# Performance work log

Hardware: AMD Instinct MI355X
Metric: run time of the kernel (lower is better)

## Reference

```python
import jax, jax.numpy as jnp
import numpy as np
from jax import lax


def setup_inputs() -> dict:
    key = jax.random.key(0)
    k0, k1, k2, k3 = jax.random.split(key, 4)
    B, Ct, Ht, Wt = 8, 16, 16, 16
    Cm, Hm, Wm = 16, 128, 128
    Cout, K = 64, 3
    template = jax.random.normal(k0, (B, Ct, Ht, Wt), jnp.float32)
    tomatch = jax.random.normal(k1, (B, Cm, Hm, Wm), jnp.float32)
    fan_in = Ct * Cm * K * K
    bound = 1.0 / np.sqrt(fan_in)
    W = jax.random.uniform(k2, (Cout, Ct * Cm, K, K), jnp.float32, -bound, bound)
    b = jax.random.uniform(k3, (Cout,), jnp.float32, -bound, bound)
    return {"template": template, "tomatch": tomatch, "W": W, "b": b}


def _dense_corr(template, tomatch):
    # template: [B, Ct, Ht, Wt], tomatch: [B, Cm, Hm, Wm]
    B, Ct, Ht, Wt = template.shape
    _, Cm, Hm, Wm = tomatch.shape
    # ReplicationPad2d((0, Wt-1, 0, Ht-1)) -> edge pad right/bottom only
    padded = jnp.pad(tomatch, ((0, 0), (0, 0), (0, Ht - 1), (0, Wt - 1)), mode="edge")

    def per_example(tm_pad, tp):
        # tm_pad: [Cm, Hm+Ht-1, Wm+Wt-1] -> treat Cm as batch with 1 channel
        # tp: [Ct, Ht, Wt] -> Ct single-channel filters
        out = lax.conv_general_dilated(
            tm_pad[:, None, :, :],  # [Cm, 1, Hp, Wp] NCHW
            tp[:, None, :, :],      # [Ct, 1, Ht, Wt] OIHW
            window_strides=(1, 1),
            padding="VALID",
        )  # [Cm, Ct, Hm, Wm] (torch conv2d = cross-correlation, same as lax)
        return out.reshape(Cm * Ct, Hm, Wm)  # channel = cm*Ct + ct, matches torch .view

    return jax.vmap(per_example)(padded, template)  # [B, Cm*Ct, Hm, Wm]


def reference(template, tomatch, W, b):
    corr = _dense_corr(template, tomatch)  # [B, Cm*Ct, Hm, Wm]
    out = lax.conv_general_dilated(corr, W, (1, 1), "SAME")  # 3x3 'same' merge conv
    return out + b[None, :, None, None]
```

## Files before the change

kernel.cpp:

```cpp
#include <hip/hip_runtime.h>
#include <hip/hip_bf16.h>


typedef __attribute__((ext_vector_type(4))) float  f32x4;
typedef __attribute__((ext_vector_type(8))) short  bf16x8;

__device__ inline unsigned int pack_bf16x2(float a, float b) {
    unsigned int ua = __builtin_bit_cast(unsigned int, a);
    unsigned int ub = __builtin_bit_cast(unsigned int, b);
    ua = (ua + 0x7fffu + ((ua >> 16) & 1u)) >> 16;
    ub = (ub + 0x7fffu + ((ub >> 16) & 1u)) >> 16;
    return ua | (ub << 16);
}
__device__ inline unsigned short cvt1(float f) {
    unsigned int u = __builtin_bit_cast(unsigned int, f);
    return (unsigned short)((u + 0x7fffu + ((u >> 16) & 1u)) >> 16);
}

__global__ __launch_bounds__(256) void corr_mfma(
    const float* __restrict__ tp, const float* __restrict__ tm,
    unsigned short* __restrict__ corrb)
{
    __shared__ __align__(16) unsigned short smA[2 * 2 * 31 * 82];

    const int t    = threadIdx.x;
    const int wave = t >> 6, lane = t & 63;
    const int n    = lane & 15, quad = lane >> 4;
    const int qh   = quad >> 1, jq = quad & 1;

    const int xh   = (int)blockIdx.x & 1;
    const int y0   = ((int)blockIdx.x >> 1) << 4;
    const int pair = (int)blockIdx.y & 7;
    const int b    = (int)blockIdx.y >> 3;
    const int xg0  = xh << 6;

    for (int cm2 = 0; cm2 < 2; ++cm2) {
        const float* src = tm + (((size_t)(b * 16 + pair * 2 + cm2)) << 14);
        for (int e = t; e < 31 * 80; e += 256) {
            int r = e / 80, c = e - r * 80;
            int gy = y0 + r;  gy = gy > 127 ? 127 : gy;
            int gx = xg0 + c; gx = gx > 127 ? 127 : gx;
            unsigned short h = cvt1(src[(gy << 7) + gx]);
            smA[((cm2 * 2 + 0) * 31 + r) * 82 + c] = h;
            if (c > 0)
                smA[((cm2 * 2 + 1) * 31 + r) * 82 + (c - 1)] = h;
        }
    }
    __syncthreads();

    bf16x8 bq[8];
    {
        const float* tpb = tp + (((size_t)(b * 16 + n)) << 8);
#pragma unroll
        for (int kc = 0; kc < 8; ++kc) {
            const float4* q = (const float4*)(tpb + (((2 * kc + qh) << 4) + (jq << 3)));
            float4 a = q[0], c4 = q[1];
            union { uint4 u; bf16x8 h; } cv;
            cv.u.x = pack_bf16x2(a.x, a.y);
            cv.u.y = pack_bf16x2(a.z, a.w);
            cv.u.z = pack_bf16x2(c4.x, c4.y);
            cv.u.w = pack_bf16x2(c4.z, c4.w);
            bq[kc] = cv.h;
        }
    }

    const unsigned* smAd = (const unsigned*)smA;
    const int PITCH = 41, PLANE = 31 * 41;

#pragma unroll 1
    for (int it = 0; it < 8; ++it) {
        const int lxa  = (wave << 4) + (it << 1);
        const int D00  = (n + qh) * PITCH + ((lxa + (jq << 3)) >> 1);

        f32x4 acc[4];
#pragma unroll
        for (int q = 0; q < 4; ++q) acc[q] = (f32x4){0.f, 0.f, 0.f, 0.f};

#pragma unroll
        for (int kc = 0; kc < 8; ++kc) {
            const int dof = D00 + kc * 82;
#pragma unroll
            for (int ch = 0; ch < 4; ++ch) {
                const int d = dof + ch * PLANE;
                union { uint4 u; bf16x8 h; } fr;
                fr.u.x = smAd[d];     fr.u.y = smAd[d + 1];
                fr.u.z = smAd[d + 2]; fr.u.w = smAd[d + 3];
                const int ai = ((ch & 1) << 1) | (ch >> 1);
                acc[ai] = __builtin_amdgcn_mfma_f32_16x16x32_bf16(
                    bq[kc], fr.h, acc[ai], 0, 0, 0);
            }
        }

        const int y = y0 + n;
#pragma unroll
        for (int ai = 0; ai < 4; ++ai) {
            const int par = ai >> 1, cm2 = ai & 1;
            const int x   = xg0 + lxa + par;
            uint2 v;
            v.x = pack_bf16x2(acc[ai][0], acc[ai][1]);
            v.y = pack_bf16x2(acc[ai][2], acc[ai][3]);
            unsigned short* dst = corrb
                + (((size_t)(b * 16384 + (y << 7) + x)) << 8)
                + (pair << 5) + (cm2 << 4) + (quad << 2);
            *(uint2*)dst = v;
        }
    }
}

__global__ __launch_bounds__(256) void wt_kernel(
    const float* __restrict__ W, unsigned short* __restrict__ Wb)
{
    int idx = (int)blockIdx.x * 256 + (int)threadIdx.x;
    int c  = idx & 255;
    int rem = idx >> 8;
    int co = rem % 64;
    int kk = rem / 64;
    Wb[idx] = cvt1(W[(size_t)co * 2304 + (size_t)c * 9 + kk]);
}

__global__ __launch_bounds__(256) void merge_mfma(
    const unsigned short* __restrict__ corrb, const unsigned short* __restrict__ Wb,
    const float* __restrict__ bias, float* __restrict__ out)
{
    __shared__ __align__(16) unsigned short sm[10 * 34 * 72];

    const int t    = threadIdx.x;
    const int wave = t >> 6, lane = t & 63;
    const int n    = lane & 15, quad = lane >> 4;
    const int x0   = (int)blockIdx.x << 5;
    const int y0   = (int)blockIdx.y << 3;
    const int b    = (int)blockIdx.z;

    f32x4 acc[4][4];
#pragma unroll
    for (int a = 0; a < 4; ++a)
#pragma unroll
        for (int q = 0; q < 4; ++q) acc[a][q] = (f32x4){0.f, 0.f, 0.f, 0.f};

    const unsigned short* cb = corrb + ((size_t)b << 22);

    uint4 v[11];

#define SLAB_LOAD(C0)                                                        \
    {                                                                        \
        _Pragma("unroll")                                                    \
        for (int k = 0; k < 11; ++k) {                                       \
            int e = t + (k << 8);                                            \
            int ci = e & 7, rem = e >> 3;                                    \
            int cc = rem % 34, r = rem / 34;                                 \
            int gy = y0 - 1 + r, gx = x0 - 1 + cc;                           \
            uint4 vv = {0u, 0u, 0u, 0u};                                     \
            if (e < 2720 && (unsigned)gy < 128u && (unsigned)gx < 128u)      \
                vv = *(const uint4*)(cb + (((size_t)((gy << 7) + gx)) << 8)  \
                                        + (C0) + (ci << 3));                 \
            v[k] = vv;                                                       \
        }                                                                    \
    }
#define SLAB_WRITE()                                                         \
    {                                                                        \
        _Pragma("unroll")                                                    \
        for (int k = 0; k < 11; ++k) {                                       \
            int e = t + (k << 8);                                            \
            int ci = e & 7, rem = e >> 3;                                    \
            int cc = rem % 34, r = rem / 34;                                 \
            if (e < 2720)                                                    \
                *(uint4*)&sm[r * 2448 + cc * 72 + (ci << 3)] = v[k];         \
        }                                                                    \
    }

    SLAB_LOAD(0)
    SLAB_WRITE()
    __syncthreads();

#pragma unroll 1
    for (int c0 = 0; c0 < 256; c0 += 64) {
        if (c0 < 192) SLAB_LOAD(c0 + 64)

        const unsigned short* wpb = Wb + (size_t)n * 256 + c0 + (quad << 3);
        bf16x8 afc[4];
        {
#pragma unroll
            for (int ct = 0; ct < 4; ++ct)
                afc[ct] = *(const bf16x8*)(wpb + (size_t)ct * 4096);
        }
#pragma unroll 1
        for (int idx = 0; idx < 18; ++idx) {
            const int nidx = idx < 17 ? idx + 1 : 17;
            const int nkk = nidx >> 1, nkc = nidx & 1;
            bf16x8 afn[4];
#pragma unroll
            for (int ct = 0; ct < 4; ++ct)
                afn[ct] = *(const bf16x8*)(wpb + (size_t)nkk * 16384
                                               + (nkc << 5) + (size_t)ct * 4096);
            const int kk = idx >> 1, kc = idx & 1;
            const int dy = kk / 3, dx = kk - 3 * dy;
#pragma unroll
            for (int nt = 0; nt < 4; ++nt) {
                const int prow = 2 * wave + (nt >> 1) + dy;
                const int pcol = ((nt & 1) << 4) + n + dx;
                bf16x8 bf = *(const bf16x8*)&sm[prow * 2448 + pcol * 72
                                                + (kc << 5) + (quad << 3)];
#pragma unroll
                for (int ct = 0; ct < 4; ++ct)
                    acc[ct][nt] = __builtin_amdgcn_mfma_f32_16x16x32_bf16(
                        afc[ct], bf, acc[ct][nt], 0, 0, 0);
            }
#pragma unroll
            for (int ct = 0; ct < 4; ++ct) afc[ct] = afn[ct];
        }

        __syncthreads();
        if (c0 < 192) SLAB_WRITE()
        __syncthreads();
    }

#pragma unroll
    for (int ct = 0; ct < 4; ++ct) {
#pragma unroll
        for (int nt = 0; nt < 4; ++nt) {
            const int y   = y0 + 2 * wave + (nt >> 1);
            const int x   = x0 + ((nt & 1) << 4) + n;
            const int co0 = (ct << 4) + (quad << 2);
            float* op = out + (((size_t)((b << 6) + co0) << 7) + y) * 128 + x;
#pragma unroll
            for (int r = 0; r < 4; ++r)
                op[(size_t)r << 14] = acc[ct][nt][r] + bias[co0 + r];
        }
    }
#undef SLAB_LOAD
#undef SLAB_WRITE
}

extern "C" void kernel_launch(void* const* d_in, const int* in_sizes, int n_in,
                              void* d_out, int out_size, void* d_ws, size_t ws_size,
                              hipStream_t stream)
{
    const float* tp   = (const float*)d_in[0];
    const float* tm   = (const float*)d_in[1];
    const float* Wt   = (const float*)d_in[2];
    const float* bias = (const float*)d_in[3];
    float* out = (float*)d_out;

    unsigned short* corrb = (unsigned short*)d_ws;
    unsigned short* Wb    = corrb + (size_t)8 * 16384 * 256;

    corr_mfma<<<dim3(16, 64), dim3(256), 0, stream>>>(tp, tm, corrb);
    wt_kernel<<<dim3(576), dim3(256), 0, stream>>>(Wt, Wb);
    merge_mfma<<<dim3(4, 16, 8), dim3(256), 0, stream>>>(corrb, Wb, bias, out);
}
```

Measured before the change: 194.1 us.

## Pre-pad tomatch into bf16 shifted planes and shrink merge tile

Adds a prep kernel that writes tomatch as edge-padded bf16 planes, with two column-parity copies, into workspace. A new correlation kernel then reads MFMA B fragments straight from global memory instead of staging through LDS. The merge kernel drops its register-prefetched double buffering for a smaller 16-wide tile with twice as many blocks, and the weight layout is reorganised for contiguous per-lane loads. This trades extra global traffic and an extra launch for fewer LDS stages and higher occupancy, and falls back to the old correlation path when the workspace is too small.

```diff
diff --git a/kernel.cpp b/kernel.cpp
--- a/kernel.cpp
+++ b/kernel.cpp
@@ -15,6 +15,191 @@
 __device__ inline unsigned short cvt1(float f) {
     unsigned int u = __builtin_bit_cast(unsigned int, f);
     return (unsigned short)((u + 0x7fffu + ((u >> 16) & 1u)) >> 16);
+}
+__device__ inline bf16x8 load16_a4(const unsigned short* p) {
+    bf16x8 v;
+    __builtin_memcpy(&v, __builtin_assume_aligned(p, 4), 16);
+    return v;
+}
+
+__global__ __launch_bounds__(256) void tmb_prep(
+    const float* __restrict__ tm, unsigned short* __restrict__ tmb)
+{
+    int idx = (int)blockIdx.x * 256 + (int)threadIdx.x;
+    int c   = idx % 144;
+    int rem = idx / 144;
+    int r   = rem % 143;  rem /= 143;
+    int cm  = rem & 15;   rem >>= 4;
+    int b   = rem & 7;
+    int p   = rem >> 3;
+    int gy = r > 127 ? 127 : r;
+    int gx = c + p; gx = gx > 127 ? 127 : gx;
+    tmb[idx] = cvt1(tm[(((size_t)(b * 16 + cm)) << 14) + (gy << 7) + gx]);
+}
+
+__global__ __launch_bounds__(256) void corr_g(
+    const float* __restrict__ tp, const unsigned short* __restrict__ tmb,
+    unsigned short* __restrict__ corrb)
+{
+    const int t    = threadIdx.x;
+    const int wave = t >> 6, lane = t & 63;
+    const int n    = lane & 15, quad = lane >> 4;
+    const int qh   = quad >> 1, jq = quad & 1;
+
+    const int y    = ((int)blockIdx.x << 2) + wave;
+    const int pair = (int)blockIdx.y & 7;
+    const int b    = (int)blockIdx.y >> 3;
+
+    bf16x8 bq[8];
+    {
+        const float* tpb = tp + (((size_t)(b * 16 + n)) << 8);
+#pragma unroll
+        for (int kc = 0; kc < 8; ++kc) {
+            const float4* q = (const float4*)(tpb + (((2 * kc + qh) << 4) + (jq << 3)));
+            float4 a = q[0], c4 = q[1];
+            union { uint4 u; bf16x8 h; } cv;
+            cv.u.x = pack_bf16x2(a.x, a.y);
+            cv.u.y = pack_bf16x2(a.z, a.w);
+            cv.u.z = pack_bf16x2(c4.x, c4.y);
+            cv.u.w = pack_bf16x2(c4.z, c4.w);
+            bq[kc] = cv.h;
+        }
+    }
+
+    const size_t PLANE = 20592;
+    const size_t PARS  = 128 * PLANE;
+    const size_t bcm0  = (size_t)(b * 16 + pair * 2) * PLANE;
+    const int    colb  = (n << 3) + (jq << 3);
+
+    f32x4 acc[2][8];
+#pragma unroll
+    for (int c2 = 0; c2 < 2; ++c2)
+#pragma unroll
+        for (int s = 0; s < 8; ++s) acc[c2][s] = (f32x4){0.f, 0.f, 0.f, 0.f};
+
+#pragma unroll 1
+    for (int kc = 0; kc < 8; ++kc) {
+        const int row = y + 2 * kc + qh;
+#pragma unroll
+        for (int c2 = 0; c2 < 2; ++c2) {
+            const unsigned short* base =
+                tmb + bcm0 + (size_t)c2 * PLANE + (size_t)row * 144 + colb;
+#pragma unroll
+            for (int s = 0; s < 8; ++s) {
+                const unsigned short* ps = base + (s & 1) * PARS + ((s >> 1) << 1);
+                bf16x8 bf = load16_a4(ps);
+                acc[c2][s] = __builtin_amdgcn_mfma_f32_16x16x32_bf16(
+                    bq[kc], bf, acc[c2][s], 0, 0, 0);
+            }
+        }
+    }
+
+    const size_t posb = ((size_t)(b * 16384 + (y << 7)) << 8) + (pair << 5);
+#pragma unroll
+    for (int s = 0; s < 8; ++s) {
+        const int x = (n << 3) + s;
+#pragma unroll
+        for (int c2 = 0; c2 < 2; ++c2) {
+            uint2 v;
+            v.x = pack_bf16x2(acc[c2][s][0], acc[c2][s][1]);
+            v.y = pack_bf16x2(acc[c2][s][2], acc[c2][s][3]);
+            *(uint2*)(corrb + posb + ((size_t)x << 8) + (c2 << 4) + (quad << 2)) = v;
+        }
+    }
+}
+
+__global__ __launch_bounds__(256) void wt_kernel(
+    const float* __restrict__ W, unsigned short* __restrict__ Wb2)
+{
+    int idx = (int)blockIdx.x * 256 + (int)threadIdx.x;
+    int ci = idx & 7;
+    int co = (idx >> 3) & 63;
+    int cb = (idx >> 9) & 31;
+    int kk = idx >> 14;
+    int c  = (cb << 3) + ci;
+    Wb2[idx] = cvt1(W[(size_t)co * 2304 + (size_t)c * 9 + kk]);
+}
+
+__global__ __launch_bounds__(256, 4) void merge_mfma(
+    const unsigned short* __restrict__ corrb, const unsigned short* __restrict__ Wb2,
+    const float* __restrict__ bias, float* __restrict__ out)
+{
+    __shared__ __align__(16) unsigned short sm[10 * 18 * 72];
+
+    const int t    = threadIdx.x;
+    const int wave = t >> 6, lane = t & 63;
+    const int n    = lane & 15, quad = lane >> 4;
+    const int x0   = (int)blockIdx.x << 4;
+    const int y0   = (int)blockIdx.y << 3;
+    const int b    = (int)blockIdx.z;
+
+    f32x4 acc[4][2];
+#pragma unroll
+    for (int a = 0; a < 4; ++a)
+#pragma unroll
+        for (int q = 0; q < 2; ++q) acc[a][q] = (f32x4){0.f, 0.f, 0.f, 0.f};
+
+    const unsigned short* cb = corrb + ((size_t)b << 22);
+
+#pragma unroll 1
+    for (int c0 = 0; c0 < 256; c0 += 64) {
+        __syncthreads();
+#pragma unroll
+        for (int k = 0; k < 6; ++k) {
+            int e = t + (k << 8);
+            if (e < 1440) {
+                int ci  = e & 7;
+                int rem = e >> 3;
+                int cc  = rem % 18, r = rem / 18;
+                int gy = y0 - 1 + r, gx = x0 - 1 + cc;
+                uint4 vv = {0u, 0u, 0u, 0u};
+                if ((unsigned)gy < 128u && (unsigned)gx < 128u)
+                    vv = *(const uint4*)(cb + (((size_t)((gy << 7) + gx)) << 8)
+                                            + c0 + (ci << 3));
+                *(uint4*)&sm[(r * 18 + cc) * 72 + (ci << 3)] = vv;
+            }
+        }
+        __syncthreads();
+
+#pragma unroll 1
+        for (int kk = 0; kk < 9; ++kk) {
+            const int dy = kk / 3, dx = kk - 3 * (kk / 3);
+#pragma unroll
+            for (int kc = 0; kc < 2; ++kc) {
+                const unsigned short* wp = Wb2
+                    + ((((size_t)kk * 32 + (c0 >> 3) + (kc << 2) + quad) << 6) + n) * 8;
+                bf16x8 af[4];
+#pragma unroll
+                for (int ct = 0; ct < 4; ++ct)
+                    af[ct] = *(const bf16x8*)(wp + (ct << 7));
+#pragma unroll
+                for (int nt = 0; nt < 2; ++nt) {
+                    const int prow = 2 * wave + nt + dy;
+                    const int pcol = n + dx;
+                    bf16x8 bf = *(const bf16x8*)&sm[(prow * 18 + pcol) * 72
+                                                    + (kc << 5) + (quad << 3)];
+#pragma unroll
+                    for (int ct = 0; ct < 4; ++ct)
+                        acc[ct][nt] = __builtin_amdgcn_mfma_f32_16x16x32_bf16(
+                            af[ct], bf, acc[ct][nt], 0, 0, 0);
+                }
+            }
+        }
+    }
+
+#pragma unroll
+    for (int ct = 0; ct < 4; ++ct) {
+#pragma unroll
+        for (int nt = 0; nt < 2; ++nt) {
+            const int y   = y0 + 2 * wave + nt;
+            const int x   = x0 + n;
+            const int co0 = (ct << 4) + (quad << 2);
+            float* op = out + (((size_t)((b << 6) + co0) << 7) + y) * 128 + x;
+#pragma unroll
+            for (int r = 0; r < 4; ++r)
+                op[(size_t)r << 14] = acc[ct][nt][r] + bias[co0 + r];
+        }
+    }
 }
 
 __global__ __launch_bounds__(256) void corr_mfma(
@@ -69,8 +254,8 @@
 
 #pragma unroll 1
     for (int it = 0; it < 8; ++it) {
-        const int lxa  = (wave << 4) + (it << 1);
-        const int D00  = (n + qh) * PITCH + ((lxa + (jq << 3)) >> 1);
+        const int lxa = (wave << 4) + (it << 1);
+        const int D00 = (n + qh) * PITCH + ((lxa + (jq << 3)) >> 1);
 
         f32x4 acc[4];
 #pragma unroll
@@ -107,130 +292,6 @@
     }
 }
 
-__global__ __launch_bounds__(256) void wt_kernel(
-    const float* __restrict__ W, unsigned short* __restrict__ Wb)
-{
-    int idx = (int)blockIdx.x * 256 + (int)threadIdx.x;
-    int c  = idx & 255;
-    int rem = idx >> 8;
-    int co = rem % 64;
-    int kk = rem / 64;
-    Wb[idx] = cvt1(W[(size_t)co * 2304 + (size_t)c * 9 + kk]);
-}
-
-__global__ __launch_bounds__(256) void merge_mfma(
-    const unsigned short* __restrict__ corrb, const unsigned short* __restrict__ Wb,
-    const float* __restrict__ bias, float* __restrict__ out)
-{
-    __shared__ __align__(16) unsigned short sm[10 * 34 * 72];
-
-    const int t    = threadIdx.x;
-    const int wave = t >> 6, lane = t & 63;
-    const int n    = lane & 15, quad = lane >> 4;
-    const int x0   = (int)blockIdx.x << 5;
-    const int y0   = (int)blockIdx.y << 3;
-    const int b    = (int)blockIdx.z;
-
-    f32x4 acc[4][4];
-#pragma unroll
-    for (int a = 0; a < 4; ++a)
-#pragma unroll
-        for (int q = 0; q < 4; ++q) acc[a][q] = (f32x4){0.f, 0.f, 0.f, 0.f};
-
-    const unsigned short* cb = corrb + ((size_t)b << 22);
-
-    uint4 v[11];
-
-#define SLAB_LOAD(C0)                                                        \
-    {                                                                        \
-        _Pragma("unroll")                                                    \
-        for (int k = 0; k < 11; ++k) {                                       \
-            int e = t + (k << 8);                                            \
-            int ci = e & 7, rem = e >> 3;                                    \
-            int cc = rem % 34, r = rem / 34;                                 \
-            int gy = y0 - 1 + r, gx = x0 - 1 + cc;                           \
-            uint4 vv = {0u, 0u, 0u, 0u};                                     \
-            if (e < 2720 && (unsigned)gy < 128u && (unsigned)gx < 128u)      \
-                vv = *(const uint4*)(cb + (((size_t)((gy << 7) + gx)) << 8)  \
-                                        + (C0) + (ci << 3));                 \
-            v[k] = vv;                                                       \
-        }                                                                    \
-    }
-#define SLAB_WRITE()                                                         \
-    {                                                                        \
-        _Pragma("unroll")                                                    \
-        for (int k = 0; k < 11; ++k) {                                       \
-            int e = t + (k << 8);                                            \
-            int ci = e & 7, rem = e >> 3;                                    \
-            int cc = rem % 34, r = rem / 34;                                 \
-            if (e < 2720)                                                    \
-                *(uint4*)&sm[r * 2448 + cc * 72 + (ci << 3)] = v[k];         \
-        }                                                                    \
-    }
-
-    SLAB_LOAD(0)
-    SLAB_WRITE()
-    __syncthreads();
-
-#pragma unroll 1
-    for (int c0 = 0; c0 < 256; c0 += 64) {
-        if (c0 < 192) SLAB_LOAD(c0 + 64)
-
-        const unsigned short* wpb = Wb + (size_t)n * 256 + c0 + (quad << 3);
-        bf16x8 afc[4];
-        {
-#pragma unroll
-            for (int ct = 0; ct < 4; ++ct)
-                afc[ct] = *(const bf16x8*)(wpb + (size_t)ct * 4096);
-        }
-#pragma unroll 1
-        for (int idx = 0; idx < 18; ++idx) {
-            const int nidx = idx < 17 ? idx + 1 : 17;
-            const int nkk = nidx >> 1, nkc = nidx & 1;
-            bf16x8 afn[4];
-#pragma unroll
-            for (int ct = 0; ct < 4; ++ct)
-                afn[ct] = *(const bf16x8*)(wpb + (size_t)nkk * 16384
-                                               + (nkc << 5) + (size_t)ct * 4096);
-            const int kk = idx >> 1, kc = idx & 1;
-            const int dy = kk / 3, dx = kk - 3 * dy;
-#pragma unroll
-            for (int nt = 0; nt < 4; ++nt) {
-                const int prow = 2 * wave + (nt >> 1) + dy;
-                const int pcol = ((nt & 1) << 4) + n + dx;
-                bf16x8 bf = *(const bf16x8*)&sm[prow * 2448 + pcol * 72
-                                                + (kc << 5) + (quad << 3)];
-#pragma unroll
-                for (int ct = 0; ct < 4; ++ct)
-                    acc[ct][nt] = __builtin_amdgcn_mfma_f32_16x16x32_bf16(
-                        afc[ct], bf, acc[ct][nt], 0, 0, 0);
-            }
-#pragma unroll
-            for (int ct = 0; ct < 4; ++ct) afc[ct] = afn[ct];
-        }
-
-        __syncthreads();
-        if (c0 < 192) SLAB_WRITE()
-        __syncthreads();
-    }
-
-#pragma unroll
-    for (int ct = 0; ct < 4; ++ct) {
-#pragma unroll
-        for (int nt = 0; nt < 4; ++nt) {
-            const int y   = y0 + 2 * wave + (nt >> 1);
-            const int x   = x0 + ((nt & 1) << 4) + n;
-            const int co0 = (ct << 4) + (quad << 2);
-            float* op = out + (((size_t)((b << 6) + co0) << 7) + y) * 128 + x;
-#pragma unroll
-            for (int r = 0; r < 4; ++r)
-                op[(size_t)r << 14] = acc[ct][nt][r] + bias[co0 + r];
-        }
-    }
-#undef SLAB_LOAD
-#undef SLAB_WRITE
-}
-
 extern "C" void kernel_launch(void* const* d_in, const int* in_sizes, int n_in,
                               void* d_out, int out_size, void* d_ws, size_t ws_size,
                               hipStream_t stream)
@@ -242,9 +303,18 @@
     float* out = (float*)d_out;
 
     unsigned short* corrb = (unsigned short*)d_ws;
-    unsigned short* Wb    = corrb + (size_t)8 * 16384 * 256;
-
-    corr_mfma<<<dim3(16, 64), dim3(256), 0, stream>>>(tp, tm, corrb);
-    wt_kernel<<<dim3(576), dim3(256), 0, stream>>>(Wt, Wb);
-    merge_mfma<<<dim3(4, 16, 8), dim3(256), 0, stream>>>(corrb, Wb, bias, out);
-}
+    unsigned short* Wb2   = corrb + (size_t)8 * 16384 * 256;
+    unsigned short* tmb   = Wb2 + (size_t)9 * 32 * 64 * 8;
+
+    const size_t need_v3 = (size_t)67108864 + 294912 + 10543104;
+    const bool use_v3 = (ws_size >= need_v3);
+
+    if (use_v3) {
+        tmb_prep<<<dim3(20592), dim3(256), 0, stream>>>(tm, tmb);
+        corr_g<<<dim3(32, 64), dim3(256), 0, stream>>>(tp, tmb, corrb);
+    } else {
+        corr_mfma<<<dim3(16, 64), dim3(256), 0, stream>>>(tp, tm, corrb);
+    }
+    wt_kernel<<<dim3(576), dim3(256), 0, stream>>>(Wt, Wb2);
+    merge_mfma<<<dim3(8, 16, 8), dim3(256), 0, stream>>>(corrb, Wb2, bias, out);
+}
```

Result: slower. 354.8 us (+82.8%).

## Pre-pad tomatch to bf16 buffer and read MFMA operands directly from global

Applied to the files above, without the earlier changes.

Adds a prep kernel that edge-pads and converts tomatch to a bf16 buffer with a 144-element row pitch. The correlation kernel drops its LDS staging and barrier and instead loads operand rows straight from global memory into registers, prefetching the next row while the current one feeds the MFMAs. It builds odd-offset operands by shifting register words, and each wave now computes a full row of 128 x positions. This trades LDS traffic and sync for an extra kernel launch, an extra global round-trip of the padded input, and more registers.

```diff
diff --git a/kernel.cpp b/kernel.cpp
--- a/kernel.cpp
+++ b/kernel.cpp
@@ -17,36 +17,32 @@
     return (unsigned short)((u + 0x7fffu + ((u >> 16) & 1u)) >> 16);
 }
 
-__global__ __launch_bounds__(256) void corr_mfma(
-    const float* __restrict__ tp, const float* __restrict__ tm,
+__global__ __launch_bounds__(256) void tmb_prep(
+    const float* __restrict__ tm, unsigned short* __restrict__ tmb)
+{
+    int idx = (int)blockIdx.x * 256 + (int)threadIdx.x;
+    if (idx >= 8 * 16 * 143 * 144) return;
+    int c   = idx % 144;
+    int rem = idx / 144;
+    int r   = rem % 143;
+    int bc  = rem / 143;
+    int gy = r > 127 ? 127 : r;
+    int gx = c > 127 ? 127 : c;
+    tmb[idx] = cvt1(tm[(((size_t)bc) << 14) + (gy << 7) + gx]);
+}
+
+__global__ __launch_bounds__(256) void corr_g2(
+    const float* __restrict__ tp, const unsigned short* __restrict__ tmb,
     unsigned short* __restrict__ corrb)
 {
-    __shared__ __align__(16) unsigned short smA[2 * 2 * 31 * 82];
-
     const int t    = threadIdx.x;
     const int wave = t >> 6, lane = t & 63;
     const int n    = lane & 15, quad = lane >> 4;
     const int qh   = quad >> 1, jq = quad & 1;
 
-    const int xh   = (int)blockIdx.x & 1;
-    const int y0   = ((int)blockIdx.x >> 1) << 4;
+    const int y    = ((int)blockIdx.x << 2) + wave;
     const int pair = (int)blockIdx.y & 7;
     const int b    = (int)blockIdx.y >> 3;
-    const int xg0  = xh << 6;
-
-    for (int cm2 = 0; cm2 < 2; ++cm2) {
-        const float* src = tm + (((size_t)(b * 16 + pair * 2 + cm2)) << 14);
-        for (int e = t; e < 31 * 80; e += 256) {
-            int r = e / 80, c = e - r * 80;
-            int gy = y0 + r;  gy = gy > 127 ? 127 : gy;
-            int gx = xg0 + c; gx = gx > 127 ? 127 : gx;
-            unsigned short h = cvt1(src[(gy << 7) + gx]);
-            smA[((cm2 * 2 + 0) * 31 + r) * 82 + c] = h;
-            if (c > 0)
-                smA[((cm2 * 2 + 1) * 31 + r) * 82 + (c - 1)] = h;
-        }
-    }
-    __syncthreads();
 
     bf16x8 bq[8];
     {
@@ -64,45 +60,67 @@
         }
     }
 
-    const unsigned* smAd = (const unsigned*)smA;
-    const int PITCH = 41, PLANE = 31 * 41;
+    const size_t PLANE = 20592;
+    const unsigned short* base0 = tmb
+        + (size_t)(b * 16 + pair * 2) * PLANE + (n << 3) + (jq << 3);
+
+    f32x4 acc[2][8];
+#pragma unroll
+    for (int c2 = 0; c2 < 2; ++c2)
+#pragma unroll
+        for (int s = 0; s < 8; ++s) acc[c2][s] = (f32x4){0.f, 0.f, 0.f, 0.f};
+
+    unsigned int w[8];
+    {
+        const uint4* p = (const uint4*)(base0 + (size_t)(y + qh) * 144);
+        uint4 lo = p[0], hi = p[1];
+        w[0] = lo.x; w[1] = lo.y; w[2] = lo.z; w[3] = lo.w;
+        w[4] = hi.x; w[5] = hi.y; w[6] = hi.z; w[7] = hi.w;
+    }
 
 #pragma unroll 1
-    for (int it = 0; it < 8; ++it) {
-        const int lxa  = (wave << 4) + (it << 1);
-        const int D00  = (n + qh) * PITCH + ((lxa + (jq << 3)) >> 1);
-
-        f32x4 acc[4];
-#pragma unroll
-        for (int q = 0; q < 4; ++q) acc[q] = (f32x4){0.f, 0.f, 0.f, 0.f};
-
-#pragma unroll
-        for (int kc = 0; kc < 8; ++kc) {
-            const int dof = D00 + kc * 82;
-#pragma unroll
-            for (int ch = 0; ch < 4; ++ch) {
-                const int d = dof + ch * PLANE;
-                union { uint4 u; bf16x8 h; } fr;
-                fr.u.x = smAd[d];     fr.u.y = smAd[d + 1];
-                fr.u.z = smAd[d + 2]; fr.u.w = smAd[d + 3];
-                const int ai = ((ch & 1) << 1) | (ch >> 1);
-                acc[ai] = __builtin_amdgcn_mfma_f32_16x16x32_bf16(
-                    bq[kc], fr.h, acc[ai], 0, 0, 0);
+    for (int u = 0; u < 16; ++u) {
+        const int kc = u >> 1, c2 = u & 1;
+        const int un = u < 15 ? u + 1 : 15;
+        unsigned int wn[8];
+        {
+            const uint4* p = (const uint4*)(base0
+                + (size_t)(un & 1) * PLANE
+                + (size_t)(y + ((un >> 1) << 1) + qh) * 144);
+            uint4 lo = p[0], hi = p[1];
+            wn[0] = lo.x; wn[1] = lo.y; wn[2] = lo.z; wn[3] = lo.w;
+            wn[4] = hi.x; wn[5] = hi.y; wn[6] = hi.z; wn[7] = hi.w;
+        }
+#pragma unroll
+        for (int s = 0; s < 8; ++s) {
+            union { uint4 u4; bf16x8 h; } f;
+            const int q = s >> 1;
+            if ((s & 1) == 0) {
+                f.u4.x = w[q]; f.u4.y = w[q + 1];
+                f.u4.z = w[q + 2]; f.u4.w = w[q + 3];
+            } else {
+                f.u4.x = (w[q] >> 16)     | (w[q + 1] << 16);
+                f.u4.y = (w[q + 1] >> 16) | (w[q + 2] << 16);
+                f.u4.z = (w[q + 2] >> 16) | (w[q + 3] << 16);
+                f.u4.w = (w[q + 3] >> 16) | (w[q + 4] << 16);
             }
-        }
-
-        const int y = y0 + n;
-#pragma unroll
-        for (int ai = 0; ai < 4; ++ai) {
-            const int par = ai >> 1, cm2 = ai & 1;
-            const int x   = xg0 + lxa + par;
+            acc[c2][s] = __builtin_amdgcn_mfma_f32_16x16x32_bf16(
+                bq[kc], f.h, acc[c2][s], 0, 0, 0);
+        }
+#pragma unroll
+        for (int i = 0; i < 8; ++i) w[i] = wn[i];
+    }
+
+    const size_t posb = ((size_t)(b * 16384 + (y << 7)) << 8) + (pair << 5);
+#pragma unroll
+    for (int s = 0; s < 8; ++s) {
+        const int x = (n << 3) + s;
+#pragma unroll
+        for (int c2 = 0; c2 < 2; ++c2) {
             uint2 v;
-            v.x = pack_bf16x2(acc[ai][0], acc[ai][1]);
-            v.y = pack_bf16x2(acc[ai][2], acc[ai][3]);
-            unsigned short* dst = corrb
-                + (((size_t)(b * 16384 + (y << 7) + x)) << 8)
-                + (pair << 5) + (cm2 << 4) + (quad << 2);
-            *(uint2*)dst = v;
+            v.x = pack_bf16x2(acc[c2][s][0], acc[c2][s][1]);
+            v.y = pack_bf16x2(acc[c2][s][2], acc[c2][s][3]);
+            *(uint2*)(corrb + posb + ((size_t)x << 8) + (c2 << 4) + (quad << 2)) = v;
         }
     }
 }
@@ -243,8 +261,10 @@
 
     unsigned short* corrb = (unsigned short*)d_ws;
     unsigned short* Wb    = corrb + (size_t)8 * 16384 * 256;
-
-    corr_mfma<<<dim3(16, 64), dim3(256), 0, stream>>>(tp, tm, corrb);
+    unsigned short* tmb   = Wb + (size_t)9 * 64 * 256;
+
+    tmb_prep<<<dim3(10296), dim3(256), 0, stream>>>(tm, tmb);
+    corr_g2<<<dim3(32, 64), dim3(256), 0, stream>>>(tp, tmb, corrb);
     wt_kernel<<<dim3(576), dim3(256), 0, stream>>>(Wt, Wb);
     merge_mfma<<<dim3(4, 16, 8), dim3(256), 0, stream>>>(corrb, Wb, bias, out);
 }
```

Measured after the change: 647.7 us. 3.34x slower.
